# Kernel optimization log

Measured on AMD Instinct MI355X. Metric: run time of the kernel, lower is better.

The kernel has to match this reference:

```python
import jax, jax.numpy as jnp
import numpy as np

NUM_EXPERTS = 64
TOP_K = 8
ALPHA = 0.001


def setup_inputs() -> dict:
    key = jax.random.key(0)
    k1, k2 = jax.random.split(key)
    hidden_states = jax.random.normal(k1, (16384, 2048), dtype=jnp.float32)
    # nn.Linear(D, E) weight has shape (E, D); init ~ N(0, 1/sqrt(D))
    weight = jax.random.normal(k2, (NUM_EXPERTS, 2048), dtype=jnp.float32) / jnp.sqrt(2048.0)
    return {"hidden_states": hidden_states, "weight": weight}


def reference(hidden_states, weight):
    # Router logits: (N, E)
    logits = jnp.einsum("nd,ed->ne", hidden_states, weight)
    scores = jax.nn.softmax(logits, axis=-1)

    # top-k (lax.top_k returns sorted values; torch used sorted=False, same set)
    topk_weights, topk_indices = jax.lax.top_k(scores, TOP_K)  # (N, K)
    topk_weights = topk_weights / jnp.sum(topk_weights, axis=-1, keepdims=True)

    # Aux load-balancing loss (training path). Instead of materializing a
    # (N, K, E) one-hot tensor, count tokens per expert with a scatter-add.
    num_tokens = hidden_states.shape[0]
    counts = jnp.zeros((NUM_EXPERTS,), dtype=jnp.float32).at[topk_indices.ravel()].add(1.0)
    tokens_per_expert = counts / (num_tokens * TOP_K)
    mean_prob = jnp.mean(scores, axis=0)  # (E,)
    aux_loss = ALPHA * NUM_EXPERTS * jnp.sum(tokens_per_expert * mean_prob)

    return topk_weights, topk_indices, aux_loss
```

## Files before the change

### kernel.cpp

```cpp
#include <hip/hip_runtime.h>
#include <hip/hip_bf16.h>

#define N_TOKENS 16384
#define DIM      2048
#define NEXP     64
#define TOPK     8
#define LOSCALE  2048.0f
#define NBLOCKS  512
#define LSTRIDE  66

typedef _Float16 half8   __attribute__((ext_vector_type(8)));
typedef float    floatx4 __attribute__((ext_vector_type(4)));

__global__ __launch_bounds__(256) void wprep_kernel(const float* __restrict__ W,
                                                    _Float16* __restrict__ Whi,
                                                    _Float16* __restrict__ Wlo) {
    int i = blockIdx.x * 256 + threadIdx.x;
    float w = W[i];
    _Float16 h = (_Float16)w;
    Whi[i] = h;
    Wlo[i] = (_Float16)((w - (float)h) * LOSCALE);
}

__global__ __launch_bounds__(256) void moe_kernel(const float* __restrict__ A,
                                                  const _Float16* __restrict__ Whi,
                                                  const _Float16* __restrict__ Wlo,
                                                  float* __restrict__ out_w,
                                                  float* __restrict__ out_i,
                                                  float* __restrict__ out_aux,
                                                  float* __restrict__ cnt_ws,
                                                  float* __restrict__ sp_ws,
                                                  unsigned int* __restrict__ ticket) {
    __shared__ float lds[4 * 32 * LSTRIDE];
    __shared__ float s_cnt[NEXP];
    __shared__ float s_sp[NEXP];
    __shared__ int   s_last;

    const int lane  = threadIdx.x & 63;
    const int wv    = threadIdx.x >> 6;
    const int row16 = lane & 15;
    const int quad  = lane >> 4;
    const int tbase = blockIdx.x * 32;
    const int kbase = wv * 512;

    if (threadIdx.x < NEXP) { s_cnt[threadIdx.x] = 0.f; s_sp[threadIdx.x] = 0.f; }

    floatx4 acc0[2][4] = {};
    floatx4 acc1[2][4] = {};

    const float* ap0 = A + (size_t)(tbase + row16) * DIM + quad * 8;
    const float* ap1 = ap0 + (size_t)16 * DIM;
    const size_t boff = (size_t)row16 * DIM + quad * 8;

    float4 ar[2][2];
    half8  bh[4], bl[4];
    ar[0][0] = *(const float4*)(ap0 + kbase);
    ar[0][1] = *(const float4*)(ap0 + kbase + 4);
    ar[1][0] = *(const float4*)(ap1 + kbase);
    ar[1][1] = *(const float4*)(ap1 + kbase + 4);
    #pragma unroll
    for (int nt = 0; nt < 4; ++nt) {
        bh[nt] = *(const half8*)(Whi + (size_t)nt * 16 * DIM + boff + kbase);
        bl[nt] = *(const half8*)(Wlo + (size_t)nt * 16 * DIM + boff + kbase);
    }

    for (int it = 0; it < 16; ++it) {
        float4 arn[2][2];
        half8  bhn[4], bln[4];
        if (it < 15) {
            int kc = kbase + (it + 1) * 32;
            arn[0][0] = *(const float4*)(ap0 + kc);
            arn[0][1] = *(const float4*)(ap0 + kc + 4);
            arn[1][0] = *(const float4*)(ap1 + kc);
            arn[1][1] = *(const float4*)(ap1 + kc + 4);
            #pragma unroll
            for (int nt = 0; nt < 4; ++nt) {
                bhn[nt] = *(const half8*)(Whi + (size_t)nt * 16 * DIM + boff + kc);
                bln[nt] = *(const half8*)(Wlo + (size_t)nt * 16 * DIM + boff + kc);
            }
        }

        half8 ah[2], al[2];
        #pragma unroll
        for (int mt = 0; mt < 2; ++mt) {
            float av[8] = {ar[mt][0].x, ar[mt][0].y, ar[mt][0].z, ar[mt][0].w,
                           ar[mt][1].x, ar[mt][1].y, ar[mt][1].z, ar[mt][1].w};
            #pragma unroll
            for (int j = 0; j < 8; ++j) {
                _Float16 h = (_Float16)av[j];
                ah[mt][j] = h;
                al[mt][j] = (_Float16)((av[j] - (float)h) * LOSCALE);
            }
        }

        #pragma unroll
        for (int mt = 0; mt < 2; ++mt)
            #pragma unroll
            for (int nt = 0; nt < 4; ++nt) {
                acc0[mt][nt] = __builtin_amdgcn_mfma_f32_16x16x32_f16(ah[mt], bh[nt], acc0[mt][nt], 0, 0, 0);
                acc1[mt][nt] = __builtin_amdgcn_mfma_f32_16x16x32_f16(ah[mt], bl[nt], acc1[mt][nt], 0, 0, 0);
                acc1[mt][nt] = __builtin_amdgcn_mfma_f32_16x16x32_f16(al[mt], bh[nt], acc1[mt][nt], 0, 0, 0);
            }

        #pragma unroll
        for (int mt = 0; mt < 2; ++mt) { ar[mt][0] = arn[mt][0]; ar[mt][1] = arn[mt][1]; }
        #pragma unroll
        for (int nt = 0; nt < 4; ++nt) { bh[nt] = bhn[nt]; bl[nt] = bln[nt]; }
    }

    const float inv = 1.0f / LOSCALE;
    #pragma unroll
    for (int mt = 0; mt < 2; ++mt)
        #pragma unroll
        for (int nt = 0; nt < 4; ++nt)
            #pragma unroll
            for (int reg = 0; reg < 4; ++reg) {
                int tok = mt * 16 + quad * 4 + reg;
                lds[(wv * 32 + tok) * LSTRIDE + nt * 16 + row16] =
                    acc0[mt][nt][reg] + acc1[mt][nt][reg] * inv;
            }
    __syncthreads();

    float sp = 0.f, cnt = 0.f;
    for (int i = 0; i < 8; ++i) {
        int t = wv * 8 + i;
        float lg = (lds[t * LSTRIDE + lane]              + lds[(32 + t) * LSTRIDE + lane])
                 + (lds[(64 + t) * LSTRIDE + lane]       + lds[(96 + t) * LSTRIDE + lane]);

        float m = lg;
        #pragma unroll
        for (int off = 32; off; off >>= 1) m = fmaxf(m, __shfl_xor(m, off));
        float e = expf(lg - m);
        float ssum = e;
        #pragma unroll
        for (int off = 32; off; off >>= 1) ssum += __shfl_xor(ssum, off);
        float score = e / ssum;
        sp += score;

        int rank = 0;
        #pragma unroll
        for (int j = 0; j < 64; ++j) {
            float sj = __shfl(score, j);
            rank += (sj > score) || (sj == score && j < lane);
        }
        bool sel = rank < TOPK;

        float v = sel ? score : 0.f;
        #pragma unroll
        for (int off = 32; off; off >>= 1) v += __shfl_xor(v, off);

        if (sel) {
            out_w[(size_t)(tbase + t) * TOPK + rank] = score / v;
            out_i[(size_t)(tbase + t) * TOPK + rank] = (float)lane;
            cnt += 1.f;
        }
    }

    atomicAdd(&s_sp[lane], sp);
    atomicAdd(&s_cnt[lane], cnt);
    __syncthreads();
    if (threadIdx.x < 64)       atomicAdd(&cnt_ws[threadIdx.x], s_cnt[threadIdx.x]);
    else if (threadIdx.x < 128) atomicAdd(&sp_ws[threadIdx.x - 64], s_sp[threadIdx.x - 64]);

    __threadfence();
    __syncthreads();
    if (threadIdx.x == 0)
        s_last = (atomicAdd(ticket, 1u) == (unsigned)(gridDim.x - 1));
    __syncthreads();
    if (s_last && threadIdx.x < 64) {
        float c = atomicAdd(&cnt_ws[threadIdx.x], 0.f);
        float p = atomicAdd(&sp_ws[threadIdx.x], 0.f);
        float v = (c / (float)(N_TOKENS * TOPK)) * (p / (float)N_TOKENS);
        #pragma unroll
        for (int off = 32; off; off >>= 1) v += __shfl_xor(v, off);
        if (threadIdx.x == 0) out_aux[0] = 0.001f * (float)NEXP * v;
    }
}

extern "C" void kernel_launch(void* const* d_in, const int* in_sizes, int n_in,
                              void* d_out, int out_size, void* d_ws, size_t ws_size,
                              hipStream_t stream) {
    const float* A = (const float*)d_in[0];
    const float* W = (const float*)d_in[1];
    float* out = (float*)d_out;

    _Float16*     whi    = (_Float16*)d_ws;
    _Float16*     wlo    = whi + (size_t)NEXP * DIM;
    float*        cnt_ws = (float*)(wlo + (size_t)NEXP * DIM);
    float*        sp_ws  = cnt_ws + NEXP;
    unsigned int* ticket = (unsigned int*)(sp_ws + NEXP);

    hipMemsetAsync(cnt_ws, 0, 2 * NEXP * sizeof(float) + sizeof(unsigned int), stream);

    hipLaunchKernelGGL(wprep_kernel, dim3(NEXP * DIM / 256), dim3(256), 0, stream,
                       W, whi, wlo);

    float* out_w = out;
    float* out_i = out + (size_t)N_TOKENS * TOPK;
    float* out_a = out + 2 * (size_t)N_TOKENS * TOPK;

    hipLaunchKernelGGL(moe_kernel, dim3(NBLOCKS), dim3(256), 0, stream,
                       A, whi, wlo, out_w, out_i, out_a, cnt_ws, sp_ws, ticket);
}
```

Baseline: 256.6 us.

## Stage split A tiles in LDS and partition experts across 512-thread waves

Replaces the per-wave K-split (each wave covering all 64 experts over a quarter of K, then a cross-wave reduction) with an output-tile split. Eight waves each own a 16-token by 16-expert tile over the full K. The hi/lo fp16 split of A is computed once per element cooperatively and staged in LDS in 128-wide K chunks, so each element is converted once rather than by each of the four waves that use it. The epilogue reduction across waves disappears, but there are now two block barriers per K chunk, the A prefetch is only one chunk deep, and each wave reads W directly from global with little reuse.

```diff
diff --git a/kernel.cpp b/kernel.cpp
--- a/kernel.cpp
+++ b/kernel.cpp
@@ -6,8 +6,10 @@
 #define NEXP     64
 #define TOPK     8
 #define LOSCALE  2048.0f
-#define NBLOCKS  512
-#define LSTRIDE  66
+#define NBLOCKS  (N_TOKENS / 32)
+#define BKC      128
+#define ASTRIDE  136
+#define LGSTRIDE 68
 
 typedef _Float16 half8   __attribute__((ext_vector_type(8)));
 typedef float    floatx4 __attribute__((ext_vector_type(4)));
@@ -22,7 +24,7 @@
     Wlo[i] = (_Float16)((w - (float)h) * LOSCALE);
 }
 
-__global__ __launch_bounds__(256) void moe_kernel(const float* __restrict__ A,
+__global__ __launch_bounds__(512) void moe_kernel(const float* __restrict__ A,
                                                   const _Float16* __restrict__ Whi,
                                                   const _Float16* __restrict__ Wlo,
                                                   float* __restrict__ out_w,
@@ -31,101 +33,88 @@
                                                   float* __restrict__ cnt_ws,
                                                   float* __restrict__ sp_ws,
                                                   unsigned int* __restrict__ ticket) {
-    __shared__ float lds[4 * 32 * LSTRIDE];
-    __shared__ float s_cnt[NEXP];
-    __shared__ float s_sp[NEXP];
-    __shared__ int   s_last;
+    __shared__ _Float16 Ahi[32 * ASTRIDE];
+    __shared__ _Float16 Alo[32 * ASTRIDE];
+    __shared__ float    lg_x[32 * LGSTRIDE];
+    __shared__ float    s_cnt[NEXP];
+    __shared__ float    s_sp[NEXP];
+    __shared__ int      s_last;
 
-    const int lane  = threadIdx.x & 63;
-    const int wv    = threadIdx.x >> 6;
+    const int tid   = threadIdx.x;
+    const int lane  = tid & 63;
+    const int wv    = tid >> 6;
+    const int slab  = wv & 3;
+    const int th    = wv >> 2;
     const int row16 = lane & 15;
     const int quad  = lane >> 4;
     const int tbase = blockIdx.x * 32;
-    const int kbase = wv * 512;
 
-    if (threadIdx.x < NEXP) { s_cnt[threadIdx.x] = 0.f; s_sp[threadIdx.x] = 0.f; }
+    if (tid < NEXP) { s_cnt[tid] = 0.f; s_sp[tid] = 0.f; }
 
-    floatx4 acc0[2][4] = {};
-    floatx4 acc1[2][4] = {};
+    const int srow = tid >> 4;
+    const int scg  = tid & 15;
+    const float* aload = A + (size_t)(tbase + srow) * DIM + scg * 8;
 
-    const float* ap0 = A + (size_t)(tbase + row16) * DIM + quad * 8;
-    const float* ap1 = ap0 + (size_t)16 * DIM;
-    const size_t boff = (size_t)row16 * DIM + quad * 8;
+    const size_t boff = (size_t)(slab * 16 + row16) * DIM + quad * 8;
+    _Float16* ahw = Ahi + srow * ASTRIDE + scg * 8;
+    _Float16* alw = Alo + srow * ASTRIDE + scg * 8;
+    const _Float16* ahr = Ahi + (th * 16 + row16) * ASTRIDE + quad * 8;
+    const _Float16* alr = Alo + (th * 16 + row16) * ASTRIDE + quad * 8;
 
-    float4 ar[2][2];
-    half8  bh[4], bl[4];
-    ar[0][0] = *(const float4*)(ap0 + kbase);
-    ar[0][1] = *(const float4*)(ap0 + kbase + 4);
-    ar[1][0] = *(const float4*)(ap1 + kbase);
-    ar[1][1] = *(const float4*)(ap1 + kbase + 4);
-    #pragma unroll
-    for (int nt = 0; nt < 4; ++nt) {
-        bh[nt] = *(const half8*)(Whi + (size_t)nt * 16 * DIM + boff + kbase);
-        bl[nt] = *(const half8*)(Wlo + (size_t)nt * 16 * DIM + boff + kbase);
-    }
+    floatx4 acc0 = {};
+    floatx4 acc1 = {};
 
-    for (int it = 0; it < 16; ++it) {
-        float4 arn[2][2];
-        half8  bhn[4], bln[4];
-        if (it < 15) {
-            int kc = kbase + (it + 1) * 32;
-            arn[0][0] = *(const float4*)(ap0 + kc);
-            arn[0][1] = *(const float4*)(ap0 + kc + 4);
-            arn[1][0] = *(const float4*)(ap1 + kc);
-            arn[1][1] = *(const float4*)(ap1 + kc + 4);
+    float4 ar0 = *(const float4*)(aload);
+    float4 ar1 = *(const float4*)(aload + 4);
+
+    for (int c = 0; c < DIM / BKC; ++c) {
+        {
+            float v[8] = {ar0.x, ar0.y, ar0.z, ar0.w, ar1.x, ar1.y, ar1.z, ar1.w};
+            half8 h, l;
             #pragma unroll
-            for (int nt = 0; nt < 4; ++nt) {
-                bhn[nt] = *(const half8*)(Whi + (size_t)nt * 16 * DIM + boff + kc);
-                bln[nt] = *(const half8*)(Wlo + (size_t)nt * 16 * DIM + boff + kc);
+            for (int j = 0; j < 8; ++j) {
+                _Float16 hh = (_Float16)v[j];
+                h[j] = hh;
+                l[j] = (_Float16)((v[j] - (float)hh) * LOSCALE);
             }
+            *(half8*)ahw = h;
+            *(half8*)alw = l;
+        }
+        __syncthreads();
+
+        if (c + 1 < DIM / BKC) {
+            ar0 = *(const float4*)(aload + (c + 1) * BKC);
+            ar1 = *(const float4*)(aload + (c + 1) * BKC + 4);
         }
 
-        half8 ah[2], al[2];
+        const _Float16* bbase = Whi + boff + c * BKC;
+        const _Float16* bbasl = Wlo + boff + c * BKC;
         #pragma unroll
-        for (int mt = 0; mt < 2; ++mt) {
-            float av[8] = {ar[mt][0].x, ar[mt][0].y, ar[mt][0].z, ar[mt][0].w,
-                           ar[mt][1].x, ar[mt][1].y, ar[mt][1].z, ar[mt][1].w};
-            #pragma unroll
-            for (int j = 0; j < 8; ++j) {
-                _Float16 h = (_Float16)av[j];
-                ah[mt][j] = h;
-                al[mt][j] = (_Float16)((av[j] - (float)h) * LOSCALE);
-            }
+        for (int kk = 0; kk < 4; ++kk) {
+            half8 bh = *(const half8*)(bbase + kk * 32);
+            half8 bl = *(const half8*)(bbasl + kk * 32);
+            half8 ah = *(const half8*)(ahr + kk * 32);
+            half8 al = *(const half8*)(alr + kk * 32);
+            acc0 = __builtin_amdgcn_mfma_f32_16x16x32_f16(ah, bh, acc0, 0, 0, 0);
+            acc1 = __builtin_amdgcn_mfma_f32_16x16x32_f16(ah, bl, acc1, 0, 0, 0);
+            acc1 = __builtin_amdgcn_mfma_f32_16x16x32_f16(al, bh, acc1, 0, 0, 0);
         }
-
-        #pragma unroll
-        for (int mt = 0; mt < 2; ++mt)
-            #pragma unroll
-            for (int nt = 0; nt < 4; ++nt) {
-                acc0[mt][nt] = __builtin_amdgcn_mfma_f32_16x16x32_f16(ah[mt], bh[nt], acc0[mt][nt], 0, 0, 0);
-                acc1[mt][nt] = __builtin_amdgcn_mfma_f32_16x16x32_f16(ah[mt], bl[nt], acc1[mt][nt], 0, 0, 0);
-                acc1[mt][nt] = __builtin_amdgcn_mfma_f32_16x16x32_f16(al[mt], bh[nt], acc1[mt][nt], 0, 0, 0);
-            }
-
-        #pragma unroll
-        for (int mt = 0; mt < 2; ++mt) { ar[mt][0] = arn[mt][0]; ar[mt][1] = arn[mt][1]; }
-        #pragma unroll
-        for (int nt = 0; nt < 4; ++nt) { bh[nt] = bhn[nt]; bl[nt] = bln[nt]; }
+        __syncthreads();
     }
 
     const float inv = 1.0f / LOSCALE;
     #pragma unroll
-    for (int mt = 0; mt < 2; ++mt)
-        #pragma unroll
-        for (int nt = 0; nt < 4; ++nt)
-            #pragma unroll
-            for (int reg = 0; reg < 4; ++reg) {
-                int tok = mt * 16 + quad * 4 + reg;
-                lds[(wv * 32 + tok) * LSTRIDE + nt * 16 + row16] =
-                    acc0[mt][nt][reg] + acc1[mt][nt][reg] * inv;
-            }
+    for (int reg = 0; reg < 4; ++reg) {
+        int tok = th * 16 + quad * 4 + reg;
+        lg_x[tok * LGSTRIDE + slab * 16 + row16] = acc0[reg] + acc1[reg] * inv;
+    }
     __syncthreads();
 
     float sp = 0.f, cnt = 0.f;
-    for (int i = 0; i < 8; ++i) {
-        int t = wv * 8 + i;
-        float lg = (lds[t * LSTRIDE + lane]              + lds[(32 + t) * LSTRIDE + lane])
-                 + (lds[(64 + t) * LSTRIDE + lane]       + lds[(96 + t) * LSTRIDE + lane]);
+    #pragma unroll
+    for (int i = 0; i < 4; ++i) {
+        int t = wv * 4 + i;
+        float lg = lg_x[t * LGSTRIDE + lane];
 
         float m = lg;
         #pragma unroll
@@ -159,21 +148,21 @@
     atomicAdd(&s_sp[lane], sp);
     atomicAdd(&s_cnt[lane], cnt);
     __syncthreads();
-    if (threadIdx.x < 64)       atomicAdd(&cnt_ws[threadIdx.x], s_cnt[threadIdx.x]);
-    else if (threadIdx.x < 128) atomicAdd(&sp_ws[threadIdx.x - 64], s_sp[threadIdx.x - 64]);
+    if (tid < 64)       atomicAdd(&cnt_ws[tid], s_cnt[tid]);
+    else if (tid < 128) atomicAdd(&sp_ws[tid - 64], s_sp[tid - 64]);
 
     __threadfence();
     __syncthreads();
-    if (threadIdx.x == 0)
+    if (tid == 0)
         s_last = (atomicAdd(ticket, 1u) == (unsigned)(gridDim.x - 1));
     __syncthreads();
-    if (s_last && threadIdx.x < 64) {
-        float c = atomicAdd(&cnt_ws[threadIdx.x], 0.f);
-        float p = atomicAdd(&sp_ws[threadIdx.x], 0.f);
-        float v = (c / (float)(N_TOKENS * TOPK)) * (p / (float)N_TOKENS);
+    if (s_last && tid < 64) {
+        float cc = atomicAdd(&cnt_ws[tid], 0.f);
+        float pp = atomicAdd(&sp_ws[tid], 0.f);
+        float v = (cc / (float)(N_TOKENS * TOPK)) * (pp / (float)N_TOKENS);
         #pragma unroll
         for (int off = 32; off; off >>= 1) v += __shfl_xor(v, off);
-        if (threadIdx.x == 0) out_aux[0] = 0.001f * (float)NEXP * v;
+        if (tid == 0) out_aux[0] = 0.001f * (float)NEXP * v;
     }
 }
 
@@ -199,6 +188,6 @@
     float* out_i = out + (size_t)N_TOKENS * TOPK;
     float* out_a = out + 2 * (size_t)N_TOKENS * TOPK;
 
-    hipLaunchKernelGGL(moe_kernel, dim3(NBLOCKS), dim3(256), 0, stream,
+    hipLaunchKernelGGL(moe_kernel, dim3(NBLOCKS), dim3(512), 0, stream,
                        A, whi, wlo, out_w, out_i, out_a, cnt_ws, sp_ws, ticket);
 }
```

Measured after the change: 298.6 us. 16.4% more time.
